# Optimization experiments

Hardware: AMD Instinct MI355X
Metric: run time of the kernel (lower is better)

## Reference

```python
import jax, jax.numpy as jnp
import numpy as np

N = 65536          # nodes
K = 12             # graph_k
CHUNK = 1024       # graph_knn_chunk (capped at 1024 in source)
WIDTH = 256        # mlp width
GWIDTH = 192       # graph width
DEPTH = 7          # mlp depth
GLAYERS = 4        # graph layers
COND = 64          # cond_dim
NUM_FF = 8         # fourier num per sigma
SIGMAS = (1.0, 10.0, 50.0)
SKIPS = (3, 6)     # residual skips
OUT_SCALE = 0.01
FF_DIM = 2 * len(SIGMAS) * NUM_FF  # 48 (sin+cos per sigma band)


def fourier_feats(x, B):
    # x: (N,3), B: (S,3,NUM_FF) -> (N, 2*S*NUM_FF)
    proj = jnp.einsum('nd,sdm->nsm', x, B).reshape(x.shape[0], -1)
    return jnp.concatenate([jnp.sin(proj), jnp.cos(proj)], axis=-1)


def knn_graph(x):
    # chunked exact kNN: mirrors _build_knn_graph (chunked cdist + top-k)
    x_sq = jnp.sum(x * x, axis=1)  # (N,)
    n = x.shape[0]
    col_ids = jnp.arange(n)

    def chunk_fn(start):
        rows = start + jnp.arange(CHUNK)
        xc = x[rows]                                   # (C,3)
        d = x_sq[rows][:, None] + x_sq[None, :] - 2.0 * (xc @ x.T)  # (C,N)
        d = jnp.maximum(d, 0.0)
        d = d + jnp.where(rows[:, None] == col_ids[None, :], 1e9, 0.0)  # exclude self
        _, idx = jax.lax.top_k(-d, K)                  # k smallest distances
        return idx

    idx = jax.lax.map(chunk_fn, jnp.arange(0, n, CHUNK))  # (n/C, C, K)
    return idx.reshape(n, K)


def setup_inputs() -> dict:
    key = jax.random.key(0)
    ks = jax.random.split(key, 16)
    g = lambda k, shape, fan: jax.random.normal(k, shape, jnp.float32) / np.sqrt(fan)
    sig = jnp.asarray(SIGMAS, jnp.float32)[:, None, None]
    return {
        'x': jax.random.normal(ks[0], (N, 3), jnp.float32),
        'cond': jax.random.normal(ks[1], (COND,), jnp.float32),
        'B': jax.random.normal(ks[2], (len(SIGMAS), 3, NUM_FF), jnp.float32) * sig,
        'W_in': g(ks[3], (FF_DIM, WIDTH), FF_DIM),
        'b_in': jnp.zeros((WIDTH,), jnp.float32),
        'Wg_in': g(ks[4], (FF_DIM, GWIDTH), FF_DIM),
        'bg_in': jnp.zeros((GWIDTH,), jnp.float32),
        'Ws': g(ks[5], (GLAYERS, GWIDTH, GWIDTH), GWIDTH),
        'Wn': g(ks[6], (GLAYERS, GWIDTH, GWIDTH), GWIDTH),
        'bg': jnp.zeros((GLAYERS, GWIDTH), jnp.float32),
        'Wg_out': g(ks[7], (GWIDTH, WIDTH), GWIDTH),
        'W': g(ks[8], (DEPTH, WIDTH, WIDTH), WIDTH),
        'bmlp': jnp.zeros((DEPTH, WIDTH), jnp.float32),
        'Wf_g': g(ks[9], (DEPTH, COND, WIDTH), COND),
        'bf_g': jnp.zeros((DEPTH, WIDTH), jnp.float32),
        'Wf_b': g(ks[10], (DEPTH, COND, WIDTH), COND),
        'bf_b': jnp.zeros((DEPTH, WIDTH), jnp.float32),
        'W_out': g(ks[11], (WIDTH, 3), WIDTH),
        'b_out': jnp.zeros((3,), jnp.float32),
    }


def reference(x, cond, B, W_in, b_in, Wg_in, bg_in, Ws, Wn, bg, Wg_out,
              W, bmlp, Wf_g, bf_g, Wf_b, bf_b, W_out, b_out):
    act = jax.nn.silu
    knn_idx = knn_graph(x)                     # (N,K) graph structure
    ff = fourier_feats(x, B)                   # (N,48)
    h0 = act(ff @ W_in + b_in)                 # (N,256) coordinate embedding

    # graph message-passing branch (row-normalized 1/K adjacency == neighbor mean)
    gfeat = act(ff @ Wg_in + bg_in)            # (N,192)
    for l in range(GLAYERS):
        agg = jnp.mean(gfeat[knn_idx], axis=1)  # sparse spmm: gather + mean
        gfeat = act(gfeat @ Ws[l] + agg @ Wn[l] + bg[l])

    h = h0 + gfeat @ Wg_out                    # inject graph context

    # FiLM-conditioned residual MLP trunk
    for l in range(DEPTH):
        gamma = cond @ Wf_g[l] + bf_g[l]       # (256,)
        beta = cond @ Wf_b[l] + bf_b[l]
        h = act((h @ W[l] + bmlp[l]) * (1.0 + gamma) + beta)
        if (l + 1) in SKIPS:
            h = h + h0

    return (h @ W_out + b_out) * OUT_SCALE     # (N,3) displacement
```

## Files before the change

kernel.cpp:

```cpp
#include <hip/hip_runtime.h>
#include <math.h>

#define NN      65536
#define KNN     12
#define WIDTH   256
#define GW      192
#define DEPTH   7
#define GLAYERS 4
#define FF      48

#define GC    192
#define GC3   7077888
#define GLO   (-6.0f)
#define GCW   0.0625f
#define GINV  16.0f

#define GS     128
#define GS3    2097152
#define GSINV  10.666666667f
#define CS2    0.09375f

#define QL    16

typedef __attribute__((ext_vector_type(8))) _Float16 half8;
typedef __attribute__((ext_vector_type(4))) _Float16 half4;
typedef __attribute__((ext_vector_type(4))) float    f4;

__device__ __forceinline__ float silu_f(float v) { return v / (1.0f + expf(-v)); }

#define KSWAP(A,B,IA,IB) do { if (B < A) { float _t=A; A=B; B=_t; int _u=IA; IA=IB; IB=_u; } } while(0)
#define KINSERT(DV,IV) do { b11=(DV); j11=(IV); \
    KSWAP(b10,b11,j10,j11); KSWAP(b9,b10,j9,j10); KSWAP(b8,b9,j8,j9); \
    KSWAP(b7,b8,j7,j8);  KSWAP(b6,b7,j6,j7);  KSWAP(b5,b6,j5,j6); \
    KSWAP(b4,b5,j4,j5);  KSWAP(b3,b4,j3,j4);  KSWAP(b2,b3,j2,j3); \
    KSWAP(b1,b2,j1,j2);  KSWAP(b0,b1,j0,j1); } while(0)

__global__ __launch_bounds__(256) void prep_xw_kernel(const float* __restrict__ x,
                                                      float4* __restrict__ xw) {
    int i = blockIdx.x * 256 + threadIdx.x;
    float a = x[3*i], b = x[3*i+1], c = x[3*i+2];
    xw[i] = make_float4(a, b, c, a*a + b*b + c*c);
}

__global__ __launch_bounds__(256) void zero_cnt_kernel(int* __restrict__ cnt) {
    int g = blockIdx.x*256 + threadIdx.x;
    *(int4*)&cnt[g*4] = make_int4(0,0,0,0);
}

__device__ __forceinline__ int cell_of(float v) {
    int c = (int)floorf((v - GLO) * GINV);
    return min(max(c, 0), GC-1);
}

__device__ __forceinline__ int cell2(float v) {
    int c = (int)floorf((v - GLO) * GSINV);
    return min(max(c, 0), GS-1);
}

__global__ __launch_bounds__(256) void hist_kernel(const float4* __restrict__ xw,
                                                   int* __restrict__ cnt) {
    int i = blockIdx.x*256 + threadIdx.x;
    float4 p = xw[i];
    atomicAdd(&cnt[(cell_of(p.z)*GC + cell_of(p.y))*GC + cell_of(p.x)], 1);
}

__global__ __launch_bounds__(256) void satx_kernel(int* __restrict__ S) {
    int zy = blockIdx.x*256 + threadIdx.x;
    int base = zy * GC, run = 0;
    for (int i = 0; i < GC; ++i) { run += S[base+i]; S[base+i] = run; }
}
__global__ __launch_bounds__(256) void saty_kernel(int* __restrict__ S) {
    int t = blockIdx.x*256 + threadIdx.x;
    int z = t / GC, xx = t % GC, run = 0;
    for (int y = 0; y < GC; ++y) { int idx = (z*GC + y)*GC + xx; run += S[idx]; S[idx] = run; }
}
__global__ __launch_bounds__(256) void satz_kernel(int* __restrict__ S) {
    int t = blockIdx.x*256 + threadIdx.x;
    int y = t / GC, xx = t % GC, run = 0;
    for (int z = 0; z < GC; ++z) { int idx = (z*GC + y)*GC + xx; run += S[idx]; S[idx] = run; }
}

__device__ __forceinline__ int satv(const int* __restrict__ S, int xx, int y, int z) {
    if (xx < 0 || y < 0 || z < 0) return 0;
    return S[(z*GC + y)*GC + xx];
}

__global__ __launch_bounds__(256) void seed_kernel(const float4* __restrict__ xw,
                                                   const int* __restrict__ S,
                                                   float* __restrict__ seed) {
    int q = blockIdx.x*256 + threadIdx.x;
    float4 me = xw[q];
    int cx = cell_of(me.x), cy = cell_of(me.y), cz = cell_of(me.z);
    for (int R = 1; R < GC; ++R) {
        int x0 = max(cx-R, 0), x1 = min(cx+R, GC-1);
        int y0 = max(cy-R, 0), y1 = min(cy+R, GC-1);
        int z0 = max(cz-R, 0), z1 = min(cz+R, GC-1);
        int c = satv(S,x1,y1,z1) - satv(S,x0-1,y1,z1) - satv(S,x1,y0-1,z1) - satv(S,x1,y1,z0-1)
              + satv(S,x0-1,y0-1,z1) + satv(S,x0-1,y1,z0-1) + satv(S,x1,y0-1,z0-1)
              - satv(S,x0-1,y0-1,z0-1);
        if (c >= KNN + 1) {
            float dx = fmaxf(me.x - (GLO + x0*GCW), (GLO + (x1+1)*GCW) - me.x);
            float dy = fmaxf(me.y - (GLO + y0*GCW), (GLO + (y1+1)*GCW) - me.y);
            float dz = fmaxf(me.z - (GLO + z0*GCW), (GLO + (z1+1)*GCW) - me.z);
            seed[q] = (dx*dx + dy*dy + dz*dz) * 1.00002f + 1e-6f;
            return;
        }
    }
    seed[q] = 3e38f;
}

__global__ __launch_bounds__(256) void zero2_kernel(int* __restrict__ cnt) {
    int g = blockIdx.x*256 + threadIdx.x;
    *(int4*)&cnt[g*4] = make_int4(0,0,0,0);
}

__global__ __launch_bounds__(256) void hist2_kernel(const float4* __restrict__ xw,
                                                    int* __restrict__ cnt) {
    int i = blockIdx.x*256 + threadIdx.x;
    float4 p = xw[i];
    atomicAdd(&cnt[(cell2(p.z)*GS + cell2(p.y))*GS + cell2(p.x)], 1);
}

__global__ __launch_bounds__(256) void scan1_kernel(const int* __restrict__ cnt,
                                                    int* __restrict__ bsum) {
    __shared__ int red[256];
    const int t = threadIdx.x;
    int4 v = ((const int4*)cnt)[blockIdx.x*256 + t];
    red[t] = v.x + v.y + v.z + v.w;
    __syncthreads();
    for (int off = 128; off > 0; off >>= 1) {
        if (t < off) red[t] += red[t + off];
        __syncthreads();
    }
    if (t == 0) bsum[blockIdx.x] = red[0];
}

__global__ __launch_bounds__(256) void scan2_kernel(int* __restrict__ bsum) {
    __shared__ int red[256];
    const int t = threadIdx.x;
    int v[8]; int s = 0;
#pragma unroll
    for (int i = 0; i < 8; ++i) { v[i] = bsum[t*8 + i]; s += v[i]; }
    red[t] = s;
    __syncthreads();
    for (int off = 1; off < 256; off <<= 1) {
        int x = (t >= off) ? red[t - off] : 0;
        __syncthreads();
        red[t] += x;
        __syncthreads();
    }
    int run = red[t] - s;
#pragma unroll
    for (int i = 0; i < 8; ++i) { int c = v[i]; bsum[t*8 + i] = run; run += c; }
}

__global__ __launch_bounds__(256) void scan3_kernel(int* __restrict__ cnt,
                                                    const int* __restrict__ bsum) {
    __shared__ int red[256];
    const int t = threadIdx.x;
    int4 v = ((const int4*)cnt)[blockIdx.x*256 + t];
    int s = v.x + v.y + v.z + v.w;
    red[t] = s;
    __syncthreads();
    for (int off = 1; off < 256; off <<= 1) {
        int x = (t >= off) ? red[t - off] : 0;
        __syncthreads();
        red[t] += x;
        __syncthreads();
    }
    int run = bsum[blockIdx.x] + red[t] - s;
    int4 o;
    o.x = run; run += v.x;
    o.y = run; run += v.y;
    o.z = run; run += v.z;
    o.w = run;
    ((int4*)cnt)[blockIdx.x*256 + t] = o;
}

__global__ __launch_bounds__(256) void scatter_kernel(const float4* __restrict__ xw,
                                                      int* __restrict__ cstart,
                                                      float4* __restrict__ sxw,
                                                      int* __restrict__ sid) {
    int i = blockIdx.x*256 + threadIdx.x;
    float4 p = xw[i];
    int cid = (cell2(p.z)*GS + cell2(p.y))*GS + cell2(p.x);
    int pos = atomicAdd(&cstart[cid], 1);
    sxw[pos] = p;
    sid[pos] = i;
}

#define MROUND(M) do { \
    float pb0=__shfl_xor(b0,M), pb1=__shfl_xor(b1,M), pb2=__shfl_xor(b2,M), \
          pb3=__shfl_xor(b3,M), pb4=__shfl_xor(b4,M), pb5=__shfl_xor(b5,M), \
          pb6=__shfl_xor(b6,M), pb7=__shfl_xor(b7,M), pb8=__shfl_xor(b8,M), \
          pb9=__shfl_xor(b9,M), pb10=__shfl_xor(b10,M), pb11=__shfl_xor(b11,M); \
    int  pj0=__shfl_xor(j0,M), pj1=__shfl_xor(j1,M), pj2=__shfl_xor(j2,M), \
         pj3=__shfl_xor(j3,M), pj4=__shfl_xor(j4,M), pj5=__shfl_xor(j5,M), \
         pj6=__shfl_xor(j6,M), pj7=__shfl_xor(j7,M), pj8=__shfl_xor(j8,M), \
         pj9=__shfl_xor(j9,M), pj10=__shfl_xor(j10,M), pj11=__shfl_xor(j11,M); \
    if (pb0  < b11) KINSERT(pb0, pj0);   if (pb1  < b11) KINSERT(pb1, pj1); \
    if (pb2  < b11) KINSERT(pb2, pj2);   if (pb3  < b11) KINSERT(pb3, pj3); \
    if (pb4  < b11) KINSERT(pb4, pj4);   if (pb5  < b11) KINSERT(pb5, pj5); \
    if (pb6  < b11) KINSERT(pb6, pj6);   if (pb7  < b11) KINSERT(pb7, pj7); \
    if (pb8  < b11) KINSERT(pb8, pj8);   if (pb9  < b11) KINSERT(pb9, pj9); \
    if (pb10 < b11) KINSERT(pb10, pj10); if (pb11 < b11) KINSERT(pb11, pj11); \
} while(0)

__global__ __launch_bounds__(256) void knn_direct_kernel(const float4* __restrict__ sxw,
                                                         const int* __restrict__ sid,
                                                         const int* __restrict__ cend,
                                                         const float* __restrict__ seed,
                                                         int* __restrict__ knn_idx) {
    const int gtid = blockIdx.x*256 + threadIdx.x;
    const int p   = gtid >> 4;
    const int sub = gtid & (QL-1);
    const float4 me = sxw[p];
    const int q = sid[p];
    const float qsq = me.w;
    const float rr = seed[q] + 1e-3f;
    const float r = sqrtf(rr);
    const int y0 = cell2(me.y - r), y1 = cell2(me.y + r);
    const int z0 = cell2(me.z - r), z1 = cell2(me.z + r);
    const int Wy = y1 - y0 + 1;
    const int NR = (z1 - z0 + 1) * Wy;

    float b0=3e38f,b1=3e38f,b2=3e38f,b3=3e38f,b4=3e38f,b5=3e38f,
          b6=3e38f,b7=3e38f,b8=3e38f,b9=3e38f,b10=3e38f,b11=3e38f;
    int   j0=-1,j1=-1,j2=-1,j3=-1,j4=-1,j5=-1,j6=-1,j7=-1,j8=-1,j9=-1,j10=-1,j11=-1;

    auto rowspan = [&](int rx, int& t0, int& te) {
        t0 = 0; te = 0;
        if (rx < NR) {
            int zz = z0 + rx / Wy, yy = y0 + rx % Wy;
            float ylo = (yy == 0)    ? -1e30f : GLO + yy*CS2;
            float yhi = (yy == GS-1) ?  1e30f : GLO + (yy+1)*CS2;
            float dy = fmaxf(0.0f, fmaxf(ylo - me.y, me.y - yhi));
            float zlo = (zz == 0)    ? -1e30f : GLO + zz*CS2;
            float zhi = (zz == GS-1) ?  1e30f : GLO + (zz+1)*CS2;
            float dz = fmaxf(0.0f, fmaxf(zlo - me.z, me.z - zhi));
            float rem = rr - dy*dy - dz*dz;
            if (rem > 0.0f) {
                float xr = sqrtf(rem);
                int xl = cell2(me.x - xr), xh = cell2(me.x + xr);
                int crow = (zz*GS + yy)*GS;
                int c0 = crow + xl;
                t0 = c0 ? cend[c0-1] : 0;
                te = cend[crow + xh];
            }
        }
    };

    int ri = sub;
    int t0c, tec;
    rowspan(ri, t0c, tec);
    while (ri < NR) {
        const int rn = ri + QL;
        int t0n, ten;
        rowspan(rn, t0n, ten);
        for (int t = t0c; t < tec; ++t) {
            float4 c = sxw[t];
            float dot = me.x*c.x + me.y*c.y + me.z*c.z;
            float d = fmaf(-2.0f, dot, qsq + c.w);
            d = fmaxf(d, 0.0f);
            if (d < rr && d < b11 && t != p) KINSERT(d, t);
        }
        ri = rn; t0c = t0n; tec = ten;
    }
    MROUND(1); MROUND(2); MROUND(4); MROUND(8);
    if (sub == 0) {
        knn_idx[q*KNN+0]=sid[j0];  knn_idx[q*KNN+1]=sid[j1];  knn_idx[q*KNN+2]=sid[j2];
        knn_idx[q*KNN+3]=sid[j3];  knn_idx[q*KNN+4]=sid[j4];  knn_idx[q*KNN+5]=sid[j5];
        knn_idx[q*KNN+6]=sid[j6];  knn_idx[q*KNN+7]=sid[j7];  knn_idx[q*KNN+8]=sid[j8];
        knn_idx[q*KNN+9]=sid[j9];  knn_idx[q*KNN+10]=sid[j10]; knn_idx[q*KNN+11]=sid[j11];
    }
}

__global__ __launch_bounds__(256) void convert_Wt_kernel(const float* __restrict__ W,
                                                         _Float16* __restrict__ Wt) {
    int e = blockIdx.x*256 + threadIdx.x;
    int l = e >> 16, r = e & 65535;
    int n = r >> 8, k = r & 255;
    Wt[(size_t)l*65536 + n*256 + k] = (_Float16)W[(size_t)l*65536 + k*256 + n];
}

__global__ __launch_bounds__(256) void convert_Bg_kernel(const float* __restrict__ Ws,
                                                         const float* __restrict__ Wn,
                                                         _Float16* __restrict__ Bg) {
    int e = blockIdx.x*256 + threadIdx.x;
    int l = e / 73728, r = e % 73728;
    int n = r / 384, k = r % 384;
    float v = (k < 192) ? Ws[(size_t)l*36864 + k*192 + n]
                        : Wn[(size_t)l*36864 + (k-192)*192 + n];
    Bg[(size_t)l*73728 + (size_t)n*384 + k] = (_Float16)v;
}

__global__ __launch_bounds__(256) void convert_Wgo_kernel(const float* __restrict__ Wg_out,
                                                          _Float16* __restrict__ Wgo) {
    int e = blockIdx.x*256 + threadIdx.x;
    int n = e / 192, k = e % 192;
    Wgo[e] = (_Float16)Wg_out[k*256 + n];
}

__global__ __launch_bounds__(256) void convert_Win_kernel(const float* __restrict__ W_in,
                                                          const float* __restrict__ Wg_in,
                                                          _Float16* __restrict__ WinT,
                                                          _Float16* __restrict__ WginT) {
    int e = blockIdx.x*256 + threadIdx.x;
    if (e < 16384) {
        int n = e >> 6, k = e & 63;
        WinT[e] = (_Float16)(k < FF ? W_in[k*WIDTH + n] : 0.0f);
    } else {
        int e2 = e - 16384;
        int n = e2 >> 6, k = e2 & 63;
        WginT[e2] = (_Float16)(k < FF ? Wg_in[k*GW + n] : 0.0f);
    }
}

__global__ __launch_bounds__(256) void ff_kernel(const float* __restrict__ x,
                                                 const float* __restrict__ Bf,
                                                 _Float16* __restrict__ fft) {
    const int n = blockIdx.x * 256 + threadIdx.x;
    const float x0 = x[3*n], x1 = x[3*n+1], x2 = x[3*n+2];
    _Float16 v[64];
#pragma unroll
    for (int sm = 0; sm < 24; ++sm) {
        int s = sm >> 3, m = sm & 7;
        float p = x0*Bf[s*24 + m] + x1*Bf[s*24 + 8 + m] + x2*Bf[s*24 + 16 + m];
        float sv, cv; sincosf(p, &sv, &cv);
        v[sm] = (_Float16)sv; v[24 + sm] = (_Float16)cv;
    }
#pragma unroll
    for (int k = 48; k < 64; ++k) v[k] = (_Float16)0.0f;
#pragma unroll
    for (int k8 = 0; k8 < 8; ++k8)
        *(half8*)&fft[(size_t)n*64 + k8*8] = *(half8*)&v[k8*8];
}

__global__ __launch_bounds__(192) void gather_mean_kernel(const _Float16* __restrict__ g,
                                                          const int* __restrict__ idx,
                                                          _Float16* __restrict__ agg) {
    __shared__ int nb[KNN];
    const int n = blockIdx.x;
    if (threadIdx.x < KNN) nb[threadIdx.x] = idx[n*KNN + threadIdx.x];
    __syncthreads();
    float acc = 0.0f;
#pragma unroll
    for (int k = 0; k < KNN; ++k) acc += (float)g[(size_t)nb[k]*GW + threadIdx.x];
    agg[(size_t)n*GW + threadIdx.x] = (_Float16)(acc * (1.0f/12.0f));
}

__global__ __launch_bounds__(256) void film_kernel(const float* __restrict__ cond,
                                                   const float* __restrict__ Wf_g,
                                                   const float* __restrict__ bf_g,
                                                   const float* __restrict__ Wf_b,
                                                   const float* __restrict__ bf_b,
                                                   float* __restrict__ film) {
    const int l = blockIdx.x, j = threadIdx.x;
    float g = bf_g[l*WIDTH + j], b = bf_b[l*WIDTH + j];
    for (int c = 0; c < 64; ++c) {
        float cv = cond[c];
        g = fmaf(cv, Wf_g[(size_t)(l*64 + c)*WIDTH + j], g);
        b = fmaf(cv, Wf_b[(size_t)(l*64 + c)*WIDTH + j], b);
    }
    film[l*2*WIDTH + j]         = 1.0f + g;
    film[l*2*WIDTH + WIDTH + j] = b;
}

template<int EPI>
__global__ __launch_bounds__(256) void gemm_mfma(
    const _Float16* __restrict__ A1, const _Float16* __restrict__ A2,
    const _Float16* __restrict__ Bt, int K1, int Ktot, int NC,
    const float* __restrict__ bias, const float* __restrict__ film,
    const _Float16* __restrict__ h0, _Float16* __restrict__ C, int addSkip) {
    __shared__ _Float16 As[128*40];
    __shared__ _Float16 Bs[64*40];
    const int tid = threadIdx.x;
    const int bm = blockIdx.x * 128, bn = blockIdx.y * 64;
    const int wid = tid >> 6, lane = tid & 63;
    const int wm = (wid & 1) * 64, wn = (wid >> 1) * 32;
    const int m16 = lane & 15, kq = lane >> 4;
    const int ar = tid >> 1, ah = tid & 1;
    const int br = tid >> 2, bq = tid & 3;
    f4 acc[4][2];
#pragma unroll
    for (int i = 0; i < 4; ++i)
#pragma unroll
        for (int j = 0; j < 2; ++j) acc[i][j] = (f4){0.f, 0.f, 0.f, 0.f};

    for (int kc = 0; kc < Ktot; kc += 32) {
        const _Float16* Asrc; int kl, ldA;
        if (kc < K1) { Asrc = A1; kl = kc;      ldA = K1; }
        else         { Asrc = A2; kl = kc - K1; ldA = Ktot - K1; }
        {
            const float4* src = (const float4*)&Asrc[(size_t)(bm + ar)*ldA + kl + ah*16];
            *(float4*)&As[ar*40 + ah*16]     = src[0];
            *(float4*)&As[ar*40 + ah*16 + 8] = src[1];
        }
        *(float4*)&Bs[br*40 + bq*8] = *(const float4*)&Bt[(size_t)(bn + br)*Ktot + kc + bq*8];
        __syncthreads();
        half8 af[4], bf[2];
#pragma unroll
        for (int mt = 0; mt < 4; ++mt) af[mt] = *(half8*)&As[(wm + mt*16 + m16)*40 + kq*8];
#pragma unroll
        for (int nt = 0; nt < 2; ++nt) bf[nt] = *(half8*)&Bs[(wn + nt*16 + m16)*40 + kq*8];
#pragma unroll
        for (int mt = 0; mt < 4; ++mt)
#pragma unroll
            for (int nt = 0; nt < 2; ++nt)
                acc[mt][nt] = __builtin_amdgcn_mfma_f32_16x16x32_f16(af[mt], bf[nt], acc[mt][nt], 0, 0, 0);
        __syncthreads();
    }

#pragma unroll
    for (int mt = 0; mt < 4; ++mt) {
#pragma unroll
        for (int nt = 0; nt < 2; ++nt) {
            int col = bn + wn + nt*16 + m16;
#pragma unroll
            for (int r = 0; r < 4; ++r) {
                int row = bm + wm + mt*16 + kq*4 + r;
                float v = acc[mt][nt][r];
                if (EPI == 0) {
                    v = silu_f(v + bias[col]);
                } else if (EPI == 1) {
                    v = fmaf(v + bias[col], film[col], film[NC + col]);
                    v = silu_f(v);
                    if (addSkip) v += (float)h0[(size_t)row*NC + col];
                } else {
                    v += (float)h0[(size_t)row*NC + col];
                }
                C[(size_t)row*NC + col] = (_Float16)v;
            }
        }
    }
}

__global__ __launch_bounds__(256) void out_kernel(const _Float16* __restrict__ h,
                                                  const float* __restrict__ W_out,
                                                  const float* __restrict__ b_out,
                                                  float* __restrict__ out) {
    const int n = blockIdx.x * 256 + threadIdx.x;
    float a0 = 0.f, a1 = 0.f, a2 = 0.f;
#pragma unroll 4
    for (int k8 = 0; k8 < WIDTH/8; ++k8) {
        half8 v = *(const half8*)&h[(size_t)n*WIDTH + k8*8];
#pragma unroll
        for (int u = 0; u < 8; ++u) {
            float f = (float)v[u]; int k = k8*8 + u;
            a0 = fmaf(f, W_out[k*3+0], a0);
            a1 = fmaf(f, W_out[k*3+1], a1);
            a2 = fmaf(f, W_out[k*3+2], a2);
        }
    }
    out[n*3+0] = (a0 + b_out[0]) * 0.01f;
    out[n*3+1] = (a1 + b_out[1]) * 0.01f;
    out[n*3+2] = (a2 + b_out[2]) * 0.01f;
}

extern "C" void kernel_launch(void* const* d_in, const int* in_sizes, int n_in,
                              void* d_out, int out_size, void* d_ws, size_t ws_size,
                              hipStream_t stream) {
    const float* x      = (const float*)d_in[0];
    const float* cond   = (const float*)d_in[1];
    const float* Bf     = (const float*)d_in[2];
    const float* W_in   = (const float*)d_in[3];
    const float* b_in   = (const float*)d_in[4];
    const float* Wg_in  = (const float*)d_in[5];
    const float* bg_in  = (const float*)d_in[6];
    const float* Ws     = (const float*)d_in[7];
    const float* Wn     = (const float*)d_in[8];
    const float* bg     = (const float*)d_in[9];
    const float* Wg_out = (const float*)d_in[10];
    const float* W      = (const float*)d_in[11];
    const float* bmlp   = (const float*)d_in[12];
    const float* Wf_g   = (const float*)d_in[13];
    const float* bf_g   = (const float*)d_in[14];
    const float* Wf_b   = (const float*)d_in[15];
    const float* bf_b   = (const float*)d_in[16];
    const float* W_out  = (const float*)d_in[17];
    const float* b_out  = (const float*)d_in[18];
    float* out = (float*)d_out;

    char* ws = (char*)d_ws;
    int*       knn_idx = (int*)      (ws + 0);
    float4*    xw      = (float4*)   (ws + 3145728);
    _Float16*  WinT    = (_Float16*) (ws + 3145728);
    _Float16*  WginT   = (_Float16*) (ws + 3178496);
    float*     film    = (float*)    (ws + 4194304);
    _Float16*  Bg_t    = (_Float16*) (ws + 4210688);
    _Float16*  Wgo_t   = (_Float16*) (ws + 4800512);
    _Float16*  Wt      = (_Float16*) (ws + 4898816);
    _Float16*  h0      = (_Float16*) (ws + 5816320);
    int*       cnt     = (int*)      (ws + 5816320);
    float*     seed    = (float*)    (ws + 34127872);
    _Float16*  g_a     = (_Float16*) (ws + 39370752);
    int*       cellCnt = (int*)      (ws + 39370752);
    int*       bsum    = (int*)      (ws + 47759360);
    float4*    sxw     = (float4*)   (ws + 47767552);
    int*       sid     = (int*)      (ws + 48816128);
    _Float16*  g_b     = (_Float16*) (ws + 64536576);
    _Float16*  agg     = (_Float16*) (ws + 89702400);
    _Float16*  hA      = (_Float16*) (ws + 114868224);
    _Float16*  hB      = (_Float16*) (ws + 148422656);
    _Float16*  fft     = (_Float16*) (ws + 148422656);

    prep_xw_kernel<<<NN/256, 256, 0, stream>>>(x, xw);
    zero_cnt_kernel<<<GC3/1024, 256, 0, stream>>>(cnt);
    hist_kernel<<<NN/256, 256, 0, stream>>>(xw, cnt);
    satx_kernel<<<GC*GC/256, 256, 0, stream>>>(cnt);
    saty_kernel<<<GC*GC/256, 256, 0, stream>>>(cnt);
    satz_kernel<<<GC*GC/256, 256, 0, stream>>>(cnt);
    seed_kernel<<<NN/256, 256, 0, stream>>>(xw, cnt, seed);

    zero2_kernel<<<GS3/1024, 256, 0, stream>>>(cellCnt);
    hist2_kernel<<<NN/256, 256, 0, stream>>>(xw, cellCnt);
    scan1_kernel<<<GS3/1024, 256, 0, stream>>>(cellCnt, bsum);
    scan2_kernel<<<1, 256, 0, stream>>>(bsum);
    scan3_kernel<<<GS3/1024, 256, 0, stream>>>(cellCnt, bsum);
    scatter_kernel<<<NN/256, 256, 0, stream>>>(xw, cellCnt, sxw, sid);
    knn_direct_kernel<<<NN*QL/256, 256, 0, stream>>>(sxw, sid, cellCnt, seed, knn_idx);

    film_kernel<<<DEPTH, 256, 0, stream>>>(cond, Wf_g, bf_g, Wf_b, bf_b, film);
    convert_Wt_kernel<<<DEPTH*65536/256, 256, 0, stream>>>(W, Wt);
    convert_Bg_kernel<<<GLAYERS*73728/256, 256, 0, stream>>>(Ws, Wn, Bg_t);
    convert_Wgo_kernel<<<256*192/256, 256, 0, stream>>>(Wg_out, Wgo_t);
    convert_Win_kernel<<<28672/256, 256, 0, stream>>>(W_in, Wg_in, WinT, WginT);
    ff_kernel<<<NN/256, 256, 0, stream>>>(x, Bf, fft);
    gemm_mfma<0><<<dim3(NN/128, WIDTH/64), 256, 0, stream>>>(
        fft, nullptr, WinT, 64, 64, WIDTH, b_in, nullptr, nullptr, h0, 0);
    gemm_mfma<0><<<dim3(NN/128, GW/64), 256, 0, stream>>>(
        fft, nullptr, WginT, 64, 64, GW, bg_in, nullptr, nullptr, g_a, 0);

    _Float16* gin = g_a; _Float16* gout = g_b;
    for (int l = 0; l < GLAYERS; ++l) {
        gather_mean_kernel<<<NN, GW, 0, stream>>>(gin, knn_idx, agg);
        gemm_mfma<0><<<dim3(NN/128, GW/64), 256, 0, stream>>>(
            gin, agg, Bg_t + (size_t)l*73728, GW, 2*GW, GW,
            bg + l*GW, nullptr, nullptr, gout, 0);
        _Float16* t = gin; gin = gout; gout = t;
    }
    gemm_mfma<2><<<dim3(NN/128, WIDTH/64), 256, 0, stream>>>(
        gin, nullptr, Wgo_t, GW, GW, WIDTH, nullptr, nullptr, h0, hA, 0);

    _Float16* hin = hA; _Float16* hout = hB;
    for (int l = 0; l < DEPTH; ++l) {
        int skip = (l == 2 || l == 5) ? 1 : 0;
        gemm_mfma<1><<<dim3(NN/128, WIDTH/64), 256, 0, stream>>>(
            hin, nullptr, Wt + (size_t)l*65536, WIDTH, WIDTH, WIDTH,
            bmlp + l*WIDTH, film + l*2*WIDTH, h0, hout, skip);
        _Float16* t = hin; hin = hout; hout = t;
    }
    out_kernel<<<NN/256, 256, 0, stream>>>(hin, W_out, b_out, out);
}
```

Before: 1.083 ms.

## Process nodes in spatially sorted order and vectorize neighbor gather

The whole network pipeline now runs on nodes in cell-sorted order. Features are computed from the sorted positions, kNN indices are stored as 16-bit sorted indices without remapping through sid, and the output is scattered back to the original order in out_kernel. The aim is better locality for the neighbor gathers. The gather kernel also now handles 8 nodes per block with half8 vector loads. The zero/prep/histogram kernels are fused into fewer launches, at the cost of relocating sid in the workspace and relying on 16-bit indices being enough for 65536 nodes.

After: 991.9 us. 8.4% less time.

```diff
diff --git a/kernel.cpp b/kernel.cpp
--- a/kernel.cpp
+++ b/kernel.cpp
@@ -35,18 +35,6 @@
     KSWAP(b4,b5,j4,j5);  KSWAP(b3,b4,j3,j4);  KSWAP(b2,b3,j2,j3); \
     KSWAP(b1,b2,j1,j2);  KSWAP(b0,b1,j0,j1); } while(0)
 
-__global__ __launch_bounds__(256) void prep_xw_kernel(const float* __restrict__ x,
-                                                      float4* __restrict__ xw) {
-    int i = blockIdx.x * 256 + threadIdx.x;
-    float a = x[3*i], b = x[3*i+1], c = x[3*i+2];
-    xw[i] = make_float4(a, b, c, a*a + b*b + c*c);
-}
-
-__global__ __launch_bounds__(256) void zero_cnt_kernel(int* __restrict__ cnt) {
-    int g = blockIdx.x*256 + threadIdx.x;
-    *(int4*)&cnt[g*4] = make_int4(0,0,0,0);
-}
-
 __device__ __forceinline__ int cell_of(float v) {
     int c = (int)floorf((v - GLO) * GINV);
     return min(max(c, 0), GC-1);
@@ -57,11 +45,22 @@
     return min(max(c, 0), GS-1);
 }
 
-__global__ __launch_bounds__(256) void hist_kernel(const float4* __restrict__ xw,
-                                                   int* __restrict__ cnt) {
+__global__ __launch_bounds__(256) void zero_both_kernel(int* __restrict__ cnt,
+                                                        int* __restrict__ cnt2) {
+    int g = blockIdx.x*256 + threadIdx.x;
+    if (g < GC3/4) *(int4*)&cnt[g*4] = make_int4(0,0,0,0);
+    else           *(int4*)&cnt2[(g - GC3/4)*4] = make_int4(0,0,0,0);
+}
+
+__global__ __launch_bounds__(256) void prep_hist_kernel(const float* __restrict__ x,
+                                                        float4* __restrict__ xw,
+                                                        int* __restrict__ cnt,
+                                                        int* __restrict__ cnt2) {
     int i = blockIdx.x*256 + threadIdx.x;
-    float4 p = xw[i];
-    atomicAdd(&cnt[(cell_of(p.z)*GC + cell_of(p.y))*GC + cell_of(p.x)], 1);
+    float a = x[3*i], b = x[3*i+1], c = x[3*i+2];
+    xw[i] = make_float4(a, b, c, a*a + b*b + c*c);
+    atomicAdd(&cnt[(cell_of(c)*GC + cell_of(b))*GC + cell_of(a)], 1);
+    atomicAdd(&cnt2[(cell2(c)*GS + cell2(b))*GS + cell2(a)], 1);
 }
 
 __global__ __launch_bounds__(256) void satx_kernel(int* __restrict__ S) {
@@ -109,18 +108,6 @@
     seed[q] = 3e38f;
 }
 
-__global__ __launch_bounds__(256) void zero2_kernel(int* __restrict__ cnt) {
-    int g = blockIdx.x*256 + threadIdx.x;
-    *(int4*)&cnt[g*4] = make_int4(0,0,0,0);
-}
-
-__global__ __launch_bounds__(256) void hist2_kernel(const float4* __restrict__ xw,
-                                                    int* __restrict__ cnt) {
-    int i = blockIdx.x*256 + threadIdx.x;
-    float4 p = xw[i];
-    atomicAdd(&cnt[(cell2(p.z)*GS + cell2(p.y))*GS + cell2(p.x)], 1);
-}
-
 __global__ __launch_bounds__(256) void scan1_kernel(const int* __restrict__ cnt,
                                                     int* __restrict__ bsum) {
     __shared__ int red[256];
@@ -210,14 +197,13 @@
                                                          const int* __restrict__ sid,
                                                          const int* __restrict__ cend,
                                                          const float* __restrict__ seed,
-                                                         int* __restrict__ knn_idx) {
+                                                         unsigned short* __restrict__ knn_idx) {
     const int gtid = blockIdx.x*256 + threadIdx.x;
     const int p   = gtid >> 4;
     const int sub = gtid & (QL-1);
     const float4 me = sxw[p];
-    const int q = sid[p];
     const float qsq = me.w;
-    const float rr = seed[q] + 1e-3f;
+    const float rr = seed[sid[p]] + 1e-3f;
     const float r = sqrtf(rr);
     const int y0 = cell2(me.y - r), y1 = cell2(me.y + r);
     const int z0 = cell2(me.z - r), z1 = cell2(me.z + r);
@@ -268,10 +254,12 @@
     }
     MROUND(1); MROUND(2); MROUND(4); MROUND(8);
     if (sub == 0) {
-        knn_idx[q*KNN+0]=sid[j0];  knn_idx[q*KNN+1]=sid[j1];  knn_idx[q*KNN+2]=sid[j2];
-        knn_idx[q*KNN+3]=sid[j3];  knn_idx[q*KNN+4]=sid[j4];  knn_idx[q*KNN+5]=sid[j5];
-        knn_idx[q*KNN+6]=sid[j6];  knn_idx[q*KNN+7]=sid[j7];  knn_idx[q*KNN+8]=sid[j8];
-        knn_idx[q*KNN+9]=sid[j9];  knn_idx[q*KNN+10]=sid[j10]; knn_idx[q*KNN+11]=sid[j11];
+        knn_idx[p*KNN+0]=(unsigned short)j0;  knn_idx[p*KNN+1]=(unsigned short)j1;
+        knn_idx[p*KNN+2]=(unsigned short)j2;  knn_idx[p*KNN+3]=(unsigned short)j3;
+        knn_idx[p*KNN+4]=(unsigned short)j4;  knn_idx[p*KNN+5]=(unsigned short)j5;
+        knn_idx[p*KNN+6]=(unsigned short)j6;  knn_idx[p*KNN+7]=(unsigned short)j7;
+        knn_idx[p*KNN+8]=(unsigned short)j8;  knn_idx[p*KNN+9]=(unsigned short)j9;
+        knn_idx[p*KNN+10]=(unsigned short)j10; knn_idx[p*KNN+11]=(unsigned short)j11;
     }
 }
 
@@ -316,11 +304,12 @@
     }
 }
 
-__global__ __launch_bounds__(256) void ff_kernel(const float* __restrict__ x,
+__global__ __launch_bounds__(256) void ff_kernel(const float4* __restrict__ sxw,
                                                  const float* __restrict__ Bf,
                                                  _Float16* __restrict__ fft) {
     const int n = blockIdx.x * 256 + threadIdx.x;
-    const float x0 = x[3*n], x1 = x[3*n+1], x2 = x[3*n+2];
+    const float4 pos = sxw[n];
+    const float x0 = pos.x, x1 = pos.y, x2 = pos.z;
     _Float16 v[64];
 #pragma unroll
     for (int sm = 0; sm < 24; ++sm) {
@@ -337,16 +326,25 @@
 }
 
 __global__ __launch_bounds__(192) void gather_mean_kernel(const _Float16* __restrict__ g,
-                                                          const int* __restrict__ idx,
+                                                          const unsigned short* __restrict__ idx,
                                                           _Float16* __restrict__ agg) {
-    __shared__ int nb[KNN];
-    const int n = blockIdx.x;
-    if (threadIdx.x < KNN) nb[threadIdx.x] = idx[n*KNN + threadIdx.x];
+    __shared__ unsigned short nb[8][KNN];
+    const int t = threadIdx.x;
+    const int nb8 = blockIdx.x * 8;
+    if (t < 96) { int nn = t / 12, kk = t - nn*12; nb[nn][kk] = idx[(nb8+nn)*KNN + kk]; }
     __syncthreads();
-    float acc = 0.0f;
-#pragma unroll
-    for (int k = 0; k < KNN; ++k) acc += (float)g[(size_t)nb[k]*GW + threadIdx.x];
-    agg[(size_t)n*GW + threadIdx.x] = (_Float16)(acc * (1.0f/12.0f));
+    const int nloc = t / 24, c8 = t % 24;
+    float acc[8] = {0,0,0,0,0,0,0,0};
+#pragma unroll
+    for (int k = 0; k < KNN; ++k) {
+        half8 v = *(const half8*)&g[(size_t)nb[nloc][k]*GW + c8*8];
+#pragma unroll
+        for (int u = 0; u < 8; ++u) acc[u] += (float)v[u];
+    }
+    half8 o;
+#pragma unroll
+    for (int u = 0; u < 8; ++u) o[u] = (_Float16)(acc[u] * (1.0f/12.0f));
+    *(half8*)&agg[(size_t)(nb8 + nloc)*GW + c8*8] = o;
 }
 
 __global__ __launch_bounds__(256) void film_kernel(const float* __restrict__ cond,
@@ -436,6 +434,7 @@
 }
 
 __global__ __launch_bounds__(256) void out_kernel(const _Float16* __restrict__ h,
+                                                  const int* __restrict__ sid,
                                                   const float* __restrict__ W_out,
                                                   const float* __restrict__ b_out,
                                                   float* __restrict__ out) {
@@ -452,9 +451,10 @@
             a2 = fmaf(f, W_out[k*3+2], a2);
         }
     }
-    out[n*3+0] = (a0 + b_out[0]) * 0.01f;
-    out[n*3+1] = (a1 + b_out[1]) * 0.01f;
-    out[n*3+2] = (a2 + b_out[2]) * 0.01f;
+    const int o = sid[n];
+    out[o*3+0] = (a0 + b_out[0]) * 0.01f;
+    out[o*3+1] = (a1 + b_out[1]) * 0.01f;
+    out[o*3+2] = (a2 + b_out[2]) * 0.01f;
 }
 
 extern "C" void kernel_launch(void* const* d_in, const int* in_sizes, int n_in,
@@ -482,7 +482,8 @@
     float* out = (float*)d_out;
 
     char* ws = (char*)d_ws;
-    int*       knn_idx = (int*)      (ws + 0);
+    unsigned short* knn_idx = (unsigned short*)(ws + 0);
+    int*       sid     = (int*)      (ws + 1572864);
     float4*    xw      = (float4*)   (ws + 3145728);
     _Float16*  WinT    = (_Float16*) (ws + 3145728);
     _Float16*  WginT   = (_Float16*) (ws + 3178496);
@@ -497,23 +498,19 @@
     int*       cellCnt = (int*)      (ws + 39370752);
     int*       bsum    = (int*)      (ws + 47759360);
     float4*    sxw     = (float4*)   (ws + 47767552);
-    int*       sid     = (int*)      (ws + 48816128);
     _Float16*  g_b     = (_Float16*) (ws + 64536576);
     _Float16*  agg     = (_Float16*) (ws + 89702400);
     _Float16*  hA      = (_Float16*) (ws + 114868224);
     _Float16*  hB      = (_Float16*) (ws + 148422656);
     _Float16*  fft     = (_Float16*) (ws + 148422656);
 
-    prep_xw_kernel<<<NN/256, 256, 0, stream>>>(x, xw);
-    zero_cnt_kernel<<<GC3/1024, 256, 0, stream>>>(cnt);
-    hist_kernel<<<NN/256, 256, 0, stream>>>(xw, cnt);
+    zero_both_kernel<<<(GC3+GS3)/1024, 256, 0, stream>>>(cnt, cellCnt);
+    prep_hist_kernel<<<NN/256, 256, 0, stream>>>(x, xw, cnt, cellCnt);
     satx_kernel<<<GC*GC/256, 256, 0, stream>>>(cnt);
     saty_kernel<<<GC*GC/256, 256, 0, stream>>>(cnt);
     satz_kernel<<<GC*GC/256, 256, 0, stream>>>(cnt);
     seed_kernel<<<NN/256, 256, 0, stream>>>(xw, cnt, seed);
 
-    zero2_kernel<<<GS3/1024, 256, 0, stream>>>(cellCnt);
-    hist2_kernel<<<NN/256, 256, 0, stream>>>(xw, cellCnt);
     scan1_kernel<<<GS3/1024, 256, 0, stream>>>(cellCnt, bsum);
     scan2_kernel<<<1, 256, 0, stream>>>(bsum);
     scan3_kernel<<<GS3/1024, 256, 0, stream>>>(cellCnt, bsum);
@@ -525,7 +522,7 @@
     convert_Bg_kernel<<<GLAYERS*73728/256, 256, 0, stream>>>(Ws, Wn, Bg_t);
     convert_Wgo_kernel<<<256*192/256, 256, 0, stream>>>(Wg_out, Wgo_t);
     convert_Win_kernel<<<28672/256, 256, 0, stream>>>(W_in, Wg_in, WinT, WginT);
-    ff_kernel<<<NN/256, 256, 0, stream>>>(x, Bf, fft);
+    ff_kernel<<<NN/256, 256, 0, stream>>>(sxw, Bf, fft);
     gemm_mfma<0><<<dim3(NN/128, WIDTH/64), 256, 0, stream>>>(
         fft, nullptr, WinT, 64, 64, WIDTH, b_in, nullptr, nullptr, h0, 0);
     gemm_mfma<0><<<dim3(NN/128, GW/64), 256, 0, stream>>>(
@@ -533,7 +530,7 @@
 
     _Float16* gin = g_a; _Float16* gout = g_b;
     for (int l = 0; l < GLAYERS; ++l) {
-        gather_mean_kernel<<<NN, GW, 0, stream>>>(gin, knn_idx, agg);
+        gather_mean_kernel<<<NN/8, 192, 0, stream>>>(gin, knn_idx, agg);
         gemm_mfma<0><<<dim3(NN/128, GW/64), 256, 0, stream>>>(
             gin, agg, Bg_t + (size_t)l*73728, GW, 2*GW, GW,
             bg + l*GW, nullptr, nullptr, gout, 0);
@@ -550,5 +547,5 @@
             bmlp + l*WIDTH, film + l*2*WIDTH, h0, hout, skip);
         _Float16* t = hin; hin = hout; hout = t;
     }
-    out_kernel<<<NN/256, 256, 0, stream>>>(hin, W_out, b_out, out);
-}
+    out_kernel<<<NN/256, 256, 0, stream>>>(hin, sid, W_out, b_out, out);
+}
```
